# Performance work log

Measured on AMD Instinct MI355X. Metric: run time of the kernel, lower is better.

Reference implementation:

```python
import jax, jax.numpy as jnp
import numpy as np

TOP_K = 2

def setup_inputs() -> dict:
    key = jax.random.key(0)
    k1, k2, k3, k4 = jax.random.split(key, 4)
    N, H, F, E = 2048, 1024, 2048, 8
    x = jax.random.normal(k1, (N, H), dtype=jnp.float32)
    router_weight = jax.random.normal(k2, (H, E), dtype=jnp.float32) * 0.02
    w1 = jax.random.normal(k3, (E, H, F), dtype=jnp.float32) * 0.02
    w2 = jax.random.normal(k4, (E, F, H), dtype=jnp.float32) * 0.02
    return {"x": x, "router_weight": router_weight, "w1": w1, "w2": w2}

def reference(x, router_weight, w1, w2):
    # Router: softmax over experts, top-k, renormalize (matches torch forward).
    N = x.shape[0]
    E = router_weight.shape[1]
    logits = x.astype(jnp.float32) @ router_weight            # [N, E]
    rprobs = jax.nn.softmax(logits, axis=-1)
    topk_p, topk_i = jax.lax.top_k(rprobs, TOP_K)             # [N, K]
    topk_p = topk_p / jnp.sum(topk_p, axis=-1, keepdims=True)
    # Scatter normalized top-k probs into dense [N, E] gate matrix; zeros
    # everywhere else, so gating subsumes the boolean routing_map.
    probs = jnp.zeros((N, E), dtype=jnp.float32).at[
        jnp.arange(N)[:, None], topk_i].set(topk_p)
    # Expert FFN (same math as permute -> grouped GEMM -> weighted scatter-add:
    # out[t] = sum_e probs[t,e] * gelu(x[t] @ w1[e]) @ w2[e]).
    h = jnp.einsum('nh,ehf->enf', x, w1)                      # [E, N, F]
    h = jax.nn.gelu(h, approximate=False)                     # torch F.gelu is erf-based
    y = jnp.einsum('enf,efh->enh', h, w2)                     # [E, N, H]
    out = jnp.einsum('enh,ne->nh', y, probs.astype(x.dtype))  # weighted combine
    return out
```

## Files before the change

kernel.cpp:

```cpp
#include <hip/hip_runtime.h>
#include <hip/hip_fp16.h>
#include <math.h>

#define NTOK 2048
#define HID  1024
#define FFN  2048
#define NEXP 8

#define BM 128
#define BN 128
#define BK 32
#define MAX_TILES 40

#define WS_COUNTS 0
#define WS_SEG    32
#define WS_PROBS  128
#define WS_LISTS  (128 + NTOK*NEXP*4)
#define WS_XH     262144
#define WS_W1T    (WS_XH + NTOK*HID*2)
#define WS_W2T    (WS_W1T + NEXP*HID*FFN*2)
#define WS_HBUF   (WS_W2T + NEXP*HID*FFN*2)

typedef _Float16 half8 __attribute__((ext_vector_type(8)));
typedef float    f32x4 __attribute__((ext_vector_type(4)));

static __device__ __forceinline__ unsigned short f2h_bits(float f) {
  union { _Float16 h; unsigned short u; } v;
  v.h = (_Float16)f;
  return v.u;
}
static __device__ __forceinline__ unsigned pack2(float a, float b) {
  return (unsigned)f2h_bits(a) | ((unsigned)f2h_bits(b) << 16);
}

#define GLOAD16(gsrc, ldst) \
  __builtin_amdgcn_global_load_lds( \
      (const __attribute__((address_space(1))) unsigned int*)(gsrc), \
      (__attribute__((address_space(3))) unsigned int*)(ldst), 16, 0, 0)

#define VMCNT0 asm volatile("s_waitcnt vmcnt(0)" ::: "memory")

__global__ __launch_bounds__(256) void moe_prep(
    const float* __restrict__ x, const float* __restrict__ rw,
    const float* __restrict__ w1, const float* __restrict__ w2,
    unsigned short* __restrict__ xh, unsigned short* __restrict__ w1t,
    unsigned short* __restrict__ w2t,
    int* __restrict__ counts, int* __restrict__ lists, float* __restrict__ probs)
{
  __shared__ unsigned short Ls[64][72];
  const int bid = blockIdx.x;
  const int tid = threadIdx.x;

  if (bid < 8192) {
    const float* in; unsigned short* out; int C, R, r0, c0;
    if (bid < 4096) {
      const int e = bid >> 9, rem = bid & 511;
      in = w1 + (size_t)e * HID * FFN; out = w1t + (size_t)e * HID * FFN;
      R = HID; C = FFN; c0 = (rem & 31) * 64; r0 = (rem >> 5) * 64;
    } else {
      const int b = bid - 4096, e = b >> 9, rem = b & 511;
      in = w2 + (size_t)e * HID * FFN; out = w2t + (size_t)e * HID * FFN;
      R = FFN; C = HID; c0 = (rem & 15) * 64; r0 = (rem >> 4) * 64;
    }
    {
      const int r = tid >> 2, cq = tid & 3;
      const float4* src = reinterpret_cast<const float4*>(in + (size_t)(r0 + r) * C + c0 + cq*16);
      float4 v0 = src[0], v1 = src[1], v2 = src[2], v3 = src[3];
      *reinterpret_cast<uint4*>(&Ls[r][cq*16]) =
          (uint4){pack2(v0.x,v0.y), pack2(v0.z,v0.w), pack2(v1.x,v1.y), pack2(v1.z,v1.w)};
      *reinterpret_cast<uint4*>(&Ls[r][cq*16+8]) =
          (uint4){pack2(v2.x,v2.y), pack2(v2.z,v2.w), pack2(v3.x,v3.y), pack2(v3.z,v3.w)};
    }
    __syncthreads();
    {
      const int oc = tid >> 2, rq = tid & 3;
      unsigned v[8];
#pragma unroll
      for (int j = 0; j < 8; ++j) {
        unsigned lo = Ls[rq*16 + 2*j][oc];
        unsigned hi = Ls[rq*16 + 2*j + 1][oc];
        v[j] = lo | (hi << 16);
      }
      unsigned short* dst = out + (size_t)(c0 + oc) * R + r0 + rq*16;
      *reinterpret_cast<uint4*>(dst)     = (uint4){v[0],v[1],v[2],v[3]};
      *reinterpret_cast<uint4*>(dst + 8) = (uint4){v[4],v[5],v[6],v[7]};
    }
  } else {
    const int wid = tid >> 6, lane = tid & 63;
    const int t = (bid - 8192) * 4 + wid;
    const float* xr = x + (size_t)t * HID + lane * 16;
    const float4* xp = reinterpret_cast<const float4*>(xr);
    float4 v0 = xp[0], v1 = xp[1], v2 = xp[2], v3 = xp[3];
    float xv[16] = {v0.x,v0.y,v0.z,v0.w, v1.x,v1.y,v1.z,v1.w,
                    v2.x,v2.y,v2.z,v2.w, v3.x,v3.y,v3.z,v3.w};
    float acc[NEXP];
#pragma unroll
    for (int e = 0; e < NEXP; ++e) acc[e] = 0.f;
#pragma unroll
    for (int j = 0; j < 16; ++j) {
      const float4* rp = reinterpret_cast<const float4*>(rw + (size_t)(lane*16 + j) * NEXP);
      float4 a = rp[0], b = rp[1];
      acc[0] += xv[j]*a.x; acc[1] += xv[j]*a.y; acc[2] += xv[j]*a.z; acc[3] += xv[j]*a.w;
      acc[4] += xv[j]*b.x; acc[5] += xv[j]*b.y; acc[6] += xv[j]*b.z; acc[7] += xv[j]*b.w;
    }
#pragma unroll
    for (int off = 32; off > 0; off >>= 1) {
#pragma unroll
      for (int e = 0; e < NEXP; ++e) acc[e] += __shfl_down(acc[e], off);
    }
    unsigned short* xd = xh + (size_t)t * HID + lane * 16;
    *reinterpret_cast<uint4*>(xd) =
        (uint4){pack2(v0.x,v0.y), pack2(v0.z,v0.w), pack2(v1.x,v1.y), pack2(v1.z,v1.w)};
    *reinterpret_cast<uint4*>(xd + 8) =
        (uint4){pack2(v2.x,v2.y), pack2(v2.z,v2.w), pack2(v3.x,v3.y), pack2(v3.z,v3.w)};
    if (lane == 0) {
      float m = acc[0];
#pragma unroll
      for (int e = 1; e < NEXP; ++e) m = fmaxf(m, acc[e]);
      float p[NEXP];
#pragma unroll
      for (int e = 0; e < NEXP; ++e) p[e] = expf(acc[e] - m);
      int i0 = 0;
#pragma unroll
      for (int e = 1; e < NEXP; ++e) if (p[e] > p[i0]) i0 = e;
      int i1 = -1;
#pragma unroll
      for (int e = 0; e < NEXP; ++e) {
        if (e == i0) continue;
        if (i1 < 0 || p[e] > p[i1]) i1 = e;
      }
      const float inv = 1.f / (p[i0] + p[i1]);
      probs[t * NEXP + i0] = p[i0] * inv;
      probs[t * NEXP + i1] = p[i1] * inv;
      int pos0 = atomicAdd(&counts[i0], 1); lists[i0 * NTOK + pos0] = t;
      int pos1 = atomicAdd(&counts[i1], 1); lists[i1 * NTOK + pos1] = t;
    }
  }
}

__global__ void moe_segoff(const int* __restrict__ counts, int* __restrict__ seg) {
  if (threadIdx.x == 0 && blockIdx.x == 0) {
    int run = 0;
    for (int e = 0; e < NEXP; ++e) {
      seg[e] = run;
      run += ((counts[e] + BM - 1) / BM) * BM;
    }
    seg[NEXP] = run;
  }
}

__global__ __launch_bounds__(256) void moe_gemm1(
    const unsigned short* __restrict__ xh, const unsigned short* __restrict__ w1t,
    const int* __restrict__ counts, const int* __restrict__ seg,
    const int* __restrict__ lists, unsigned short* __restrict__ hbuf)
{
  const int tile = blockIdx.x >> 4;
  const int jcol = blockIdx.x & 15;
  const int rb = tile * BM;
  if (rb >= seg[NEXP]) return;
  int e = 0;
#pragma unroll
  for (int q = 1; q < NEXP; ++q) if (seg[q] <= rb) e = q;
  const int cnt = counts[e];
  const int rloc0 = rb - seg[e];

  __shared__ int tokL[BM];
  __shared__ __align__(16) unsigned short Asm[2][BM*BK];
  __shared__ __align__(16) unsigned short Bsm[2][BM*BK];

  const int tid = threadIdx.x;
  if (tid < BM) {
    int rl = rloc0 + tid;
    tokL[tid] = (rl < cnt) ? lists[e * NTOK + rl] : 0;
  }
  __syncthreads();

  const int lane = tid & 63;
  const int wid = tid >> 6;
  const int wr = (wid >> 1) * 64;
  const int wc = (wid & 1) * 64;
  const int lr = (lane >> 4) * 4;
  const int lc = lane & 15;
  const int khi = (lane >> 4) * 8;

  const int cw8 = (lane & 3) * 8;
  const int r0 = wid*16 + (lane >> 2);
  const unsigned short* abase[2];
  const unsigned short* bbase[2];
  abase[0] = xh + (size_t)tokL[r0]      * HID + cw8;
  abase[1] = xh + (size_t)tokL[64 + r0] * HID + cw8;
  bbase[0] = w1t + ((size_t)e * FFN + jcol*BN + r0)      * HID + cw8;
  bbase[1] = w1t + ((size_t)e * FFN + jcol*BN + 64 + r0) * HID + cw8;

  f32x4 acc[4][4];
#pragma unroll
  for (int m = 0; m < 4; ++m)
#pragma unroll
    for (int n = 0; n < 4; ++n)
      acc[m][n] = (f32x4){0.f, 0.f, 0.f, 0.f};

#define STAGE1(buf, kk) do { \
    _Pragma("unroll") \
    for (int i = 0; i < 2; ++i) { \
      GLOAD16(abase[i] + (kk), &Asm[buf][(i*256 + wid*64)*8]); \
      GLOAD16(bbase[i] + (kk), &Bsm[buf][(i*256 + wid*64)*8]); \
    } } while (0)

  STAGE1(0, 0);
  VMCNT0;
  __syncthreads();
  int cur = 0;
  for (int kk = 0; kk < HID; kk += BK) {
    if (kk + BK < HID) STAGE1(cur ^ 1, kk + BK);
    half8 af[4], bf[4];
#pragma unroll
    for (int m = 0; m < 4; ++m)
      af[m] = *reinterpret_cast<const half8*>(&Asm[cur][(wr + m*16 + lc)*BK + khi]);
#pragma unroll
    for (int n = 0; n < 4; ++n)
      bf[n] = *reinterpret_cast<const half8*>(&Bsm[cur][(wc + n*16 + lc)*BK + khi]);
#pragma unroll
    for (int m = 0; m < 4; ++m)
#pragma unroll
      for (int n = 0; n < 4; ++n)
        acc[m][n] = __builtin_amdgcn_mfma_f32_16x16x32_f16(af[m], bf[n], acc[m][n], 0, 0, 0);
    VMCNT0;
    __syncthreads();
    cur ^= 1;
  }
#undef STAGE1

#pragma unroll
  for (int m = 0; m < 4; ++m) {
#pragma unroll
    for (int r = 0; r < 4; ++r) {
      unsigned short* hp = hbuf + (size_t)(rb + wr + m*16 + lr + r) * FFN + jcol*BN + wc + lc;
#pragma unroll
      for (int n = 0; n < 4; ++n) {
        float v = acc[m][n][r];
        float g = 0.5f * v * (1.f + erff(v * 0.70710678118f));
        hp[n*16] = f2h_bits(g);
      }
    }
  }
}

__global__ __launch_bounds__(256) void moe_gemm2(
    const unsigned short* __restrict__ hbuf, const unsigned short* __restrict__ w2t,
    const int* __restrict__ counts, const int* __restrict__ seg,
    const int* __restrict__ lists, const float* __restrict__ probs,
    float* __restrict__ out)
{
  const int tile = blockIdx.x >> 4;
  const int jcol = (blockIdx.x >> 1) & 7;
  const int ks   = blockIdx.x & 1;
  const int rb = tile * BM;
  if (rb >= seg[NEXP]) return;
  int e = 0;
#pragma unroll
  for (int q = 1; q < NEXP; ++q) if (seg[q] <= rb) e = q;
  const int cnt = counts[e];
  const int rloc0 = rb - seg[e];
  const int k0 = ks * (FFN / 2);
  const int k1 = k0 + (FFN / 2);

  __shared__ int tokL[BM];
  __shared__ float pL[BM];
  __shared__ __align__(16) unsigned short Asm[2][BM*BK];
  __shared__ __align__(16) unsigned short Bsm[2][BM*BK];

  const int tid = threadIdx.x;
  if (tid < BM) {
    int rl = rloc0 + tid;
    if (rl < cnt) {
      int tk = lists[e * NTOK + rl];
      tokL[tid] = tk;
      pL[tid] = probs[tk * NEXP + e];
    } else { tokL[tid] = 0; pL[tid] = 0.f; }
  }
  __syncthreads();

  const int lane = tid & 63;
  const int wid = tid >> 6;
  const int wr = (wid >> 1) * 64;
  const int wc = (wid & 1) * 64;
  const int lr = (lane >> 4) * 4;
  const int lc = lane & 15;
  const int khi = (lane >> 4) * 8;

  const int cw8 = (lane & 3) * 8;
  const int r0 = wid*16 + (lane >> 2);
  const unsigned short* abase[2];
  const unsigned short* bbase[2];
  abase[0] = hbuf + (size_t)(rb + r0)      * FFN + cw8;
  abase[1] = hbuf + (size_t)(rb + 64 + r0) * FFN + cw8;
  bbase[0] = w2t + ((size_t)e * HID + jcol*BN + r0)      * FFN + cw8;
  bbase[1] = w2t + ((size_t)e * HID + jcol*BN + 64 + r0) * FFN + cw8;

  f32x4 acc[4][4];
#pragma unroll
  for (int m = 0; m < 4; ++m)
#pragma unroll
    for (int n = 0; n < 4; ++n)
      acc[m][n] = (f32x4){0.f, 0.f, 0.f, 0.f};

#define STAGE2(buf, kk) do { \
    _Pragma("unroll") \
    for (int i = 0; i < 2; ++i) { \
      GLOAD16(abase[i] + (kk), &Asm[buf][(i*256 + wid*64)*8]); \
      GLOAD16(bbase[i] + (kk), &Bsm[buf][(i*256 + wid*64)*8]); \
    } } while (0)

  STAGE2(0, k0);
  VMCNT0;
  __syncthreads();
  int cur = 0;
  for (int kk = k0; kk < k1; kk += BK) {
    if (kk + BK < k1) STAGE2(cur ^ 1, kk + BK);
    half8 af[4], bf[4];
#pragma unroll
    for (int m = 0; m < 4; ++m)
      af[m] = *reinterpret_cast<const half8*>(&Asm[cur][(wr + m*16 + lc)*BK + khi]);
#pragma unroll
    for (int n = 0; n < 4; ++n)
      bf[n] = *reinterpret_cast<const half8*>(&Bsm[cur][(wc + n*16 + lc)*BK + khi]);
#pragma unroll
    for (int m = 0; m < 4; ++m)
#pragma unroll
      for (int n = 0; n < 4; ++n)
        acc[m][n] = __builtin_amdgcn_mfma_f32_16x16x32_f16(af[m], bf[n], acc[m][n], 0, 0, 0);
    VMCNT0;
    __syncthreads();
    cur ^= 1;
  }
#undef STAGE2

#pragma unroll
  for (int m = 0; m < 4; ++m) {
#pragma unroll
    for (int r = 0; r < 4; ++r) {
      const int lrow = wr + m*16 + lr + r;
      const int rl = rloc0 + lrow;
      if (rl >= cnt) continue;
      const int tok = tokL[lrow];
      const float p = pL[lrow];
      float* op = out + (size_t)tok * HID + jcol*BN + wc + lc;
#pragma unroll
      for (int n = 0; n < 4; ++n)
        atomicAdd(&op[n*16], p * acc[m][n][r]);
    }
  }
}

extern "C" void kernel_launch(void* const* d_in, const int* in_sizes, int n_in,
                              void* d_out, int out_size, void* d_ws, size_t ws_size,
                              hipStream_t stream) {
  const float* x  = (const float*)d_in[0];
  const float* rw = (const float*)d_in[1];
  const float* w1 = (const float*)d_in[2];
  const float* w2 = (const float*)d_in[3];
  float* out = (float*)d_out;

  char* ws = (char*)d_ws;
  int*   counts = (int*)(ws + WS_COUNTS);
  int*   seg    = (int*)(ws + WS_SEG);
  float* probs  = (float*)(ws + WS_PROBS);
  int*   lists  = (int*)(ws + WS_LISTS);
  unsigned short* xh   = (unsigned short*)(ws + WS_XH);
  unsigned short* w1t  = (unsigned short*)(ws + WS_W1T);
  unsigned short* w2t  = (unsigned short*)(ws + WS_W2T);
  unsigned short* hbuf = (unsigned short*)(ws + WS_HBUF);

  hipMemsetAsync(ws, 0, 128, stream);
  hipMemsetAsync(d_out, 0, (size_t)NTOK * HID * sizeof(float), stream);

  moe_prep<<<8192 + NTOK/4, 256, 0, stream>>>(x, rw, w1, w2, xh, w1t, w2t,
                                              counts, lists, probs);
  moe_segoff<<<1, 64, 0, stream>>>(counts, seg);
  moe_gemm1<<<MAX_TILES * (FFN / BN), 256, 0, stream>>>(xh, w1t, counts, seg, lists, hbuf);
  moe_gemm2<<<MAX_TILES * (HID / BN) * 2, 256, 0, stream>>>(hbuf, w2t, counts, seg, lists, probs, out);
}
```

Baseline: 191.8 us.

## Fuse weight fp16 conversion and transpose into GEMM B-tile loading

Removes the separate pre-pass that converted and transposed both expert weight tensors to fp16 in workspace every call. The GEMM kernels now load fp32 weight rows directly, convert with packed round-toward-zero conversion, and store transposed into a padded LDS tile. This eliminates a large read/write pass but makes each tile re-read fp32 weights and stage B through registers, with a restructured wait/sync position in the k-loop. Rounding mode changes from nearest to toward-zero for weights.

```diff
diff --git a/kernel.cpp b/kernel.cpp
--- a/kernel.cpp
+++ b/kernel.cpp
@@ -10,6 +10,7 @@
 #define BM 128
 #define BN 128
 #define BK 32
+#define LDK 36
 #define MAX_TILES 40
 
 #define WS_COUNTS 0
@@ -17,12 +18,12 @@
 #define WS_PROBS  128
 #define WS_LISTS  (128 + NTOK*NEXP*4)
 #define WS_XH     262144
-#define WS_W1T    (WS_XH + NTOK*HID*2)
-#define WS_W2T    (WS_W1T + NEXP*HID*FFN*2)
-#define WS_HBUF   (WS_W2T + NEXP*HID*FFN*2)
+#define WS_HBUF   (WS_XH + NTOK*HID*2)
 
 typedef _Float16 half8 __attribute__((ext_vector_type(8)));
+typedef __fp16   fp16x2 __attribute__((ext_vector_type(2)));
 typedef float    f32x4 __attribute__((ext_vector_type(4)));
+typedef unsigned long long u64;
 
 static __device__ __forceinline__ unsigned short f2h_bits(float f) {
   union { _Float16 h; unsigned short u; } v;
@@ -32,6 +33,11 @@
 static __device__ __forceinline__ unsigned pack2(float a, float b) {
   return (unsigned)f2h_bits(a) | ((unsigned)f2h_bits(b) << 16);
 }
+static __device__ __forceinline__ unsigned cvt2(float a, float b) {
+  union { fp16x2 h; unsigned u; } t;
+  t.h = __builtin_amdgcn_cvt_pkrtz(a, b);
+  return t.u;
+}
 
 #define GLOAD16(gsrc, ldst) \
   __builtin_amdgcn_global_load_lds( \
@@ -42,99 +48,59 @@
 
 __global__ __launch_bounds__(256) void moe_prep(
     const float* __restrict__ x, const float* __restrict__ rw,
-    const float* __restrict__ w1, const float* __restrict__ w2,
-    unsigned short* __restrict__ xh, unsigned short* __restrict__ w1t,
-    unsigned short* __restrict__ w2t,
+    unsigned short* __restrict__ xh,
     int* __restrict__ counts, int* __restrict__ lists, float* __restrict__ probs)
 {
-  __shared__ unsigned short Ls[64][72];
-  const int bid = blockIdx.x;
   const int tid = threadIdx.x;
-
-  if (bid < 8192) {
-    const float* in; unsigned short* out; int C, R, r0, c0;
-    if (bid < 4096) {
-      const int e = bid >> 9, rem = bid & 511;
-      in = w1 + (size_t)e * HID * FFN; out = w1t + (size_t)e * HID * FFN;
-      R = HID; C = FFN; c0 = (rem & 31) * 64; r0 = (rem >> 5) * 64;
-    } else {
-      const int b = bid - 4096, e = b >> 9, rem = b & 511;
-      in = w2 + (size_t)e * HID * FFN; out = w2t + (size_t)e * HID * FFN;
-      R = FFN; C = HID; c0 = (rem & 15) * 64; r0 = (rem >> 4) * 64;
-    }
-    {
-      const int r = tid >> 2, cq = tid & 3;
-      const float4* src = reinterpret_cast<const float4*>(in + (size_t)(r0 + r) * C + c0 + cq*16);
-      float4 v0 = src[0], v1 = src[1], v2 = src[2], v3 = src[3];
-      *reinterpret_cast<uint4*>(&Ls[r][cq*16]) =
-          (uint4){pack2(v0.x,v0.y), pack2(v0.z,v0.w), pack2(v1.x,v1.y), pack2(v1.z,v1.w)};
-      *reinterpret_cast<uint4*>(&Ls[r][cq*16+8]) =
-          (uint4){pack2(v2.x,v2.y), pack2(v2.z,v2.w), pack2(v3.x,v3.y), pack2(v3.z,v3.w)};
-    }
-    __syncthreads();
-    {
-      const int oc = tid >> 2, rq = tid & 3;
-      unsigned v[8];
-#pragma unroll
-      for (int j = 0; j < 8; ++j) {
-        unsigned lo = Ls[rq*16 + 2*j][oc];
-        unsigned hi = Ls[rq*16 + 2*j + 1][oc];
-        v[j] = lo | (hi << 16);
-      }
-      unsigned short* dst = out + (size_t)(c0 + oc) * R + r0 + rq*16;
-      *reinterpret_cast<uint4*>(dst)     = (uint4){v[0],v[1],v[2],v[3]};
-      *reinterpret_cast<uint4*>(dst + 8) = (uint4){v[4],v[5],v[6],v[7]};
-    }
-  } else {
-    const int wid = tid >> 6, lane = tid & 63;
-    const int t = (bid - 8192) * 4 + wid;
-    const float* xr = x + (size_t)t * HID + lane * 16;
-    const float4* xp = reinterpret_cast<const float4*>(xr);
-    float4 v0 = xp[0], v1 = xp[1], v2 = xp[2], v3 = xp[3];
-    float xv[16] = {v0.x,v0.y,v0.z,v0.w, v1.x,v1.y,v1.z,v1.w,
-                    v2.x,v2.y,v2.z,v2.w, v3.x,v3.y,v3.z,v3.w};
-    float acc[NEXP];
-#pragma unroll
-    for (int e = 0; e < NEXP; ++e) acc[e] = 0.f;
-#pragma unroll
-    for (int j = 0; j < 16; ++j) {
-      const float4* rp = reinterpret_cast<const float4*>(rw + (size_t)(lane*16 + j) * NEXP);
-      float4 a = rp[0], b = rp[1];
-      acc[0] += xv[j]*a.x; acc[1] += xv[j]*a.y; acc[2] += xv[j]*a.z; acc[3] += xv[j]*a.w;
-      acc[4] += xv[j]*b.x; acc[5] += xv[j]*b.y; acc[6] += xv[j]*b.z; acc[7] += xv[j]*b.w;
-    }
-#pragma unroll
-    for (int off = 32; off > 0; off >>= 1) {
-#pragma unroll
-      for (int e = 0; e < NEXP; ++e) acc[e] += __shfl_down(acc[e], off);
-    }
-    unsigned short* xd = xh + (size_t)t * HID + lane * 16;
-    *reinterpret_cast<uint4*>(xd) =
-        (uint4){pack2(v0.x,v0.y), pack2(v0.z,v0.w), pack2(v1.x,v1.y), pack2(v1.z,v1.w)};
-    *reinterpret_cast<uint4*>(xd + 8) =
-        (uint4){pack2(v2.x,v2.y), pack2(v2.z,v2.w), pack2(v3.x,v3.y), pack2(v3.z,v3.w)};
-    if (lane == 0) {
-      float m = acc[0];
-#pragma unroll
-      for (int e = 1; e < NEXP; ++e) m = fmaxf(m, acc[e]);
-      float p[NEXP];
-#pragma unroll
-      for (int e = 0; e < NEXP; ++e) p[e] = expf(acc[e] - m);
-      int i0 = 0;
-#pragma unroll
-      for (int e = 1; e < NEXP; ++e) if (p[e] > p[i0]) i0 = e;
-      int i1 = -1;
-#pragma unroll
-      for (int e = 0; e < NEXP; ++e) {
-        if (e == i0) continue;
-        if (i1 < 0 || p[e] > p[i1]) i1 = e;
-      }
-      const float inv = 1.f / (p[i0] + p[i1]);
-      probs[t * NEXP + i0] = p[i0] * inv;
-      probs[t * NEXP + i1] = p[i1] * inv;
-      int pos0 = atomicAdd(&counts[i0], 1); lists[i0 * NTOK + pos0] = t;
-      int pos1 = atomicAdd(&counts[i1], 1); lists[i1 * NTOK + pos1] = t;
-    }
+  const int wid = tid >> 6, lane = tid & 63;
+  const int t = blockIdx.x * 4 + wid;
+
+  const float* xr = x + (size_t)t * HID + lane * 16;
+  const float4* xp = reinterpret_cast<const float4*>(xr);
+  float4 v0 = xp[0], v1 = xp[1], v2 = xp[2], v3 = xp[3];
+  float xv[16] = {v0.x,v0.y,v0.z,v0.w, v1.x,v1.y,v1.z,v1.w,
+                  v2.x,v2.y,v2.z,v2.w, v3.x,v3.y,v3.z,v3.w};
+  float acc[NEXP];
+#pragma unroll
+  for (int e = 0; e < NEXP; ++e) acc[e] = 0.f;
+#pragma unroll
+  for (int j = 0; j < 16; ++j) {
+    const float4* rp = reinterpret_cast<const float4*>(rw + (size_t)(lane*16 + j) * NEXP);
+    float4 a = rp[0], b = rp[1];
+    acc[0] += xv[j]*a.x; acc[1] += xv[j]*a.y; acc[2] += xv[j]*a.z; acc[3] += xv[j]*a.w;
+    acc[4] += xv[j]*b.x; acc[5] += xv[j]*b.y; acc[6] += xv[j]*b.z; acc[7] += xv[j]*b.w;
+  }
+#pragma unroll
+  for (int off = 32; off > 0; off >>= 1) {
+#pragma unroll
+    for (int e = 0; e < NEXP; ++e) acc[e] += __shfl_down(acc[e], off);
+  }
+  unsigned short* xd = xh + (size_t)t * HID + lane * 16;
+  *reinterpret_cast<uint4*>(xd) =
+      (uint4){pack2(v0.x,v0.y), pack2(v0.z,v0.w), pack2(v1.x,v1.y), pack2(v1.z,v1.w)};
+  *reinterpret_cast<uint4*>(xd + 8) =
+      (uint4){pack2(v2.x,v2.y), pack2(v2.z,v2.w), pack2(v3.x,v3.y), pack2(v3.z,v3.w)};
+  if (lane == 0) {
+    float m = acc[0];
+#pragma unroll
+    for (int e = 1; e < NEXP; ++e) m = fmaxf(m, acc[e]);
+    float p[NEXP];
+#pragma unroll
+    for (int e = 0; e < NEXP; ++e) p[e] = expf(acc[e] - m);
+    int i0 = 0;
+#pragma unroll
+    for (int e = 1; e < NEXP; ++e) if (p[e] > p[i0]) i0 = e;
+    int i1 = -1;
+#pragma unroll
+    for (int e = 0; e < NEXP; ++e) {
+      if (e == i0) continue;
+      if (i1 < 0 || p[e] > p[i1]) i1 = e;
+    }
+    const float inv = 1.f / (p[i0] + p[i1]);
+    probs[t * NEXP + i0] = p[i0] * inv;
+    probs[t * NEXP + i1] = p[i1] * inv;
+    int pos0 = atomicAdd(&counts[i0], 1); lists[i0 * NTOK + pos0] = t;
+    int pos1 = atomicAdd(&counts[i1], 1); lists[i1 * NTOK + pos1] = t;
   }
 }
 
@@ -150,7 +116,7 @@
 }
 
 __global__ __launch_bounds__(256) void moe_gemm1(
-    const unsigned short* __restrict__ xh, const unsigned short* __restrict__ w1t,
+    const unsigned short* __restrict__ xh, const float* __restrict__ w1,
     const int* __restrict__ counts, const int* __restrict__ seg,
     const int* __restrict__ lists, unsigned short* __restrict__ hbuf)
 {
@@ -166,7 +132,7 @@
 
   __shared__ int tokL[BM];
   __shared__ __align__(16) unsigned short Asm[2][BM*BK];
-  __shared__ __align__(16) unsigned short Bsm[2][BM*BK];
+  __shared__ __align__(16) unsigned short Bsm[2][BN*LDK];
 
   const int tid = threadIdx.x;
   if (tid < BM) {
@@ -186,11 +152,12 @@
   const int cw8 = (lane & 3) * 8;
   const int r0 = wid*16 + (lane >> 2);
   const unsigned short* abase[2];
-  const unsigned short* bbase[2];
   abase[0] = xh + (size_t)tokL[r0]      * HID + cw8;
   abase[1] = xh + (size_t)tokL[64 + r0] * HID + cw8;
-  bbase[0] = w1t + ((size_t)e * FFN + jcol*BN + r0)      * HID + cw8;
-  bbase[1] = w1t + ((size_t)e * FFN + jcol*BN + 64 + r0) * HID + cw8;
+
+  const int kb = tid >> 5;
+  const int fb = tid & 31;
+  const float* bbase = w1 + (size_t)e * HID * FFN + (size_t)jcol * BN + fb * 4;
 
   f32x4 acc[4][4];
 #pragma unroll
@@ -199,36 +166,60 @@
     for (int n = 0; n < 4; ++n)
       acc[m][n] = (f32x4){0.f, 0.f, 0.f, 0.f};
 
-#define STAGE1(buf, kk) do { \
+  f32x4 bld[4];
+
+#define LOADB1(kk) do { \
     _Pragma("unroll") \
-    for (int i = 0; i < 2; ++i) { \
-      GLOAD16(abase[i] + (kk), &Asm[buf][(i*256 + wid*64)*8]); \
-      GLOAD16(bbase[i] + (kk), &Bsm[buf][(i*256 + wid*64)*8]); \
+    for (int j = 0; j < 4; ++j) \
+      bld[j] = *reinterpret_cast<const f32x4*>(bbase + (size_t)((kk) + kb*4 + j) * FFN); \
+  } while (0)
+
+#define STAGEA(buf, kk) do { \
+    GLOAD16(abase[0] + (kk), &Asm[buf][(wid*64)*8]); \
+    GLOAD16(abase[1] + (kk), &Asm[buf][(256 + wid*64)*8]); \
+  } while (0)
+
+#define CVTB(buf) do { \
+    _Pragma("unroll") \
+    for (int i3 = 0; i3 < 4; ++i3) { \
+      uint2 wv; \
+      wv.x = cvt2(bld[0][i3], bld[1][i3]); \
+      wv.y = cvt2(bld[2][i3], bld[3][i3]); \
+      *reinterpret_cast<uint2*>(&Bsm[buf][(fb*4 + i3)*LDK + kb*4]) = wv; \
     } } while (0)
 
-  STAGE1(0, 0);
-  VMCNT0;
-  __syncthreads();
+  LOADB1(0);
+  STAGEA(0, 0);
   int cur = 0;
   for (int kk = 0; kk < HID; kk += BK) {
-    if (kk + BK < HID) STAGE1(cur ^ 1, kk + BK);
+    CVTB(cur);
+    VMCNT0;
+    __syncthreads();
+    if (kk + BK < HID) {
+      LOADB1(kk + BK);
+      STAGEA(cur ^ 1, kk + BK);
+    }
     half8 af[4], bf[4];
 #pragma unroll
     for (int m = 0; m < 4; ++m)
       af[m] = *reinterpret_cast<const half8*>(&Asm[cur][(wr + m*16 + lc)*BK + khi]);
 #pragma unroll
-    for (int n = 0; n < 4; ++n)
-      bf[n] = *reinterpret_cast<const half8*>(&Bsm[cur][(wc + n*16 + lc)*BK + khi]);
+    for (int n = 0; n < 4; ++n) {
+      union { u64 q[2]; half8 h; } t;
+      const unsigned short* bp = &Bsm[cur][(wc + n*16 + lc)*LDK + khi];
+      t.q[0] = *reinterpret_cast<const u64*>(bp);
+      t.q[1] = *reinterpret_cast<const u64*>(bp + 4);
+      bf[n] = t.h;
+    }
 #pragma unroll
     for (int m = 0; m < 4; ++m)
 #pragma unroll
       for (int n = 0; n < 4; ++n)
         acc[m][n] = __builtin_amdgcn_mfma_f32_16x16x32_f16(af[m], bf[n], acc[m][n], 0, 0, 0);
-    VMCNT0;
-    __syncthreads();
     cur ^= 1;
   }
-#undef STAGE1
+#undef LOADB1
+#undef CVTB
 
 #pragma unroll
   for (int m = 0; m < 4; ++m) {
@@ -246,7 +237,7 @@
 }
 
 __global__ __launch_bounds__(256) void moe_gemm2(
-    const unsigned short* __restrict__ hbuf, const unsigned short* __restrict__ w2t,
+    const unsigned short* __restrict__ hbuf, const float* __restrict__ w2,
     const int* __restrict__ counts, const int* __restrict__ seg,
     const int* __restrict__ lists, const float* __restrict__ probs,
     float* __restrict__ out)
@@ -267,7 +258,7 @@
   __shared__ int tokL[BM];
   __shared__ float pL[BM];
   __shared__ __align__(16) unsigned short Asm[2][BM*BK];
-  __shared__ __align__(16) unsigned short Bsm[2][BM*BK];
+  __shared__ __align__(16) unsigned short Bsm[2][BN*LDK];
 
   const int tid = threadIdx.x;
   if (tid < BM) {
@@ -291,11 +282,12 @@
   const int cw8 = (lane & 3) * 8;
   const int r0 = wid*16 + (lane >> 2);
   const unsigned short* abase[2];
-  const unsigned short* bbase[2];
   abase[0] = hbuf + (size_t)(rb + r0)      * FFN + cw8;
   abase[1] = hbuf + (size_t)(rb + 64 + r0) * FFN + cw8;
-  bbase[0] = w2t + ((size_t)e * HID + jcol*BN + r0)      * FFN + cw8;
-  bbase[1] = w2t + ((size_t)e * HID + jcol*BN + 64 + r0) * FFN + cw8;
+
+  const int kb = tid >> 5;
+  const int fb = tid & 31;
+  const float* bbase = w2 + (size_t)e * FFN * HID + (size_t)jcol * BN + fb * 4;
 
   f32x4 acc[4][4];
 #pragma unroll
@@ -304,36 +296,56 @@
     for (int n = 0; n < 4; ++n)
       acc[m][n] = (f32x4){0.f, 0.f, 0.f, 0.f};
 
-#define STAGE2(buf, kk) do { \
+  f32x4 bld[4];
+
+#define LOADB2(kk) do { \
     _Pragma("unroll") \
-    for (int i = 0; i < 2; ++i) { \
-      GLOAD16(abase[i] + (kk), &Asm[buf][(i*256 + wid*64)*8]); \
-      GLOAD16(bbase[i] + (kk), &Bsm[buf][(i*256 + wid*64)*8]); \
+    for (int j = 0; j < 4; ++j) \
+      bld[j] = *reinterpret_cast<const f32x4*>(bbase + (size_t)((kk) + kb*4 + j) * HID); \
+  } while (0)
+
+#define CVTB(buf) do { \
+    _Pragma("unroll") \
+    for (int i3 = 0; i3 < 4; ++i3) { \
+      uint2 wv; \
+      wv.x = cvt2(bld[0][i3], bld[1][i3]); \
+      wv.y = cvt2(bld[2][i3], bld[3][i3]); \
+      *reinterpret_cast<uint2*>(&Bsm[buf][(fb*4 + i3)*LDK + kb*4]) = wv; \
     } } while (0)
 
-  STAGE2(0, k0);
-  VMCNT0;
-  __syncthreads();
+  LOADB2(k0);
+  STAGEA(0, k0);
   int cur = 0;
   for (int kk = k0; kk < k1; kk += BK) {
-    if (kk + BK < k1) STAGE2(cur ^ 1, kk + BK);
+    CVTB(cur);
+    VMCNT0;
+    __syncthreads();
+    if (kk + BK < k1) {
+      LOADB2(kk + BK);
+      STAGEA(cur ^ 1, kk + BK);
+    }
     half8 af[4], bf[4];
 #pragma unroll
     for (int m = 0; m < 4; ++m)
       af[m] = *reinterpret_cast<const half8*>(&Asm[cur][(wr + m*16 + lc)*BK + khi]);
 #pragma unroll
-    for (int n = 0; n < 4; ++n)
-      bf[n] = *reinterpret_cast<const half8*>(&Bsm[cur][(wc + n*16 + lc)*BK + khi]);
+    for (int n = 0; n < 4; ++n) {
+      union { u64 q[2]; half8 h; } t;
+      const unsigned short* bp = &Bsm[cur][(wc + n*16 + lc)*LDK + khi];
+      t.q[0] = *reinterpret_cast<const u64*>(bp);
+      t.q[1] = *reinterpret_cast<const u64*>(bp + 4);
+      bf[n] = t.h;
+    }
 #pragma unroll
     for (int m = 0; m < 4; ++m)
 #pragma unroll
       for (int n = 0; n < 4; ++n)
         acc[m][n] = __builtin_amdgcn_mfma_f32_16x16x32_f16(af[m], bf[n], acc[m][n], 0, 0, 0);
-    VMCNT0;
-    __syncthreads();
     cur ^= 1;
   }
-#undef STAGE2
+#undef LOADB2
+#undef CVTB
+#undef STAGEA
 
 #pragma unroll
   for (int m = 0; m < 4; ++m) {
@@ -367,16 +379,13 @@
   float* probs  = (float*)(ws + WS_PROBS);
   int*   lists  = (int*)(ws + WS_LISTS);
   unsigned short* xh   = (unsigned short*)(ws + WS_XH);
-  unsigned short* w1t  = (unsigned short*)(ws + WS_W1T);
-  unsigned short* w2t  = (unsigned short*)(ws + WS_W2T);
   unsigned short* hbuf = (unsigned short*)(ws + WS_HBUF);
 
   hipMemsetAsync(ws, 0, 128, stream);
   hipMemsetAsync(d_out, 0, (size_t)NTOK * HID * sizeof(float), stream);
 
-  moe_prep<<<8192 + NTOK/4, 256, 0, stream>>>(x, rw, w1, w2, xh, w1t, w2t,
-                                              counts, lists, probs);
+  moe_prep<<<NTOK/4, 256, 0, stream>>>(x, rw, xh, counts, lists, probs);
   moe_segoff<<<1, 64, 0, stream>>>(counts, seg);
-  moe_gemm1<<<MAX_TILES * (FFN / BN), 256, 0, stream>>>(xh, w1t, counts, seg, lists, hbuf);
-  moe_gemm2<<<MAX_TILES * (HID / BN) * 2, 256, 0, stream>>>(hbuf, w2t, counts, seg, lists, probs, out);
-}
+  moe_gemm1<<<MAX_TILES * 16, 256, 0, stream>>>(xh, w1, counts, seg, lists, hbuf);
+  moe_gemm2<<<MAX_TILES * 8 * 2, 256, 0, stream>>>(hbuf, w2, counts, seg, lists, probs, out);
+}
```

Measured after the change: 176.2 us. -8.1%, faster.
